# Performance work log

Hardware: AMD Instinct MI355X
Metric: run time of the kernel (lower is better)

## Reference

```python
import jax, jax.numpy as jnp
import numpy as np

EMBED_DIM = 256
NUM_HEADS = 4
LN_EPS = 1e-5


def setup_inputs() -> dict:
    b, n, e = 2, 4096, EMBED_DIM
    key = jax.random.key(0)
    ks = jax.random.split(key, 12)
    x = jax.random.normal(ks[0], (b, n, e), dtype=jnp.float32)
    # rotary cache: cos/sin of random angles, shape [2, b, n, e, 1]
    ang = jax.random.uniform(ks[1], (b, n, e, 1), dtype=jnp.float32) * (2 * np.pi)
    encoding = jnp.stack([jnp.cos(ang), jnp.sin(ang)], axis=0)
    s_e = 1.0 / np.sqrt(e)
    s_2e = 1.0 / np.sqrt(2 * e)
    Wqkv_w = jax.random.normal(ks[2], (3 * e, e), dtype=jnp.float32) * s_e
    Wqkv_b = jax.random.normal(ks[3], (3 * e,), dtype=jnp.float32) * s_e
    out_w = jax.random.normal(ks[4], (e, e), dtype=jnp.float32) * s_e
    out_b = jax.random.normal(ks[5], (e,), dtype=jnp.float32) * s_e
    ffn1_w = jax.random.normal(ks[6], (2 * e, 2 * e), dtype=jnp.float32) * s_2e
    ffn1_b = jax.random.normal(ks[7], (2 * e,), dtype=jnp.float32) * s_2e
    ln_g = jnp.ones((2 * e,), dtype=jnp.float32)
    ln_b = jnp.zeros((2 * e,), dtype=jnp.float32)
    ffn2_w = jax.random.normal(ks[8], (e, 2 * e), dtype=jnp.float32) * s_2e
    ffn2_b = jax.random.normal(ks[9], (e,), dtype=jnp.float32) * s_2e
    return {"x": x, "encoding": encoding, "Wqkv_w": Wqkv_w, "Wqkv_b": Wqkv_b,
            "out_w": out_w, "out_b": out_b, "ffn1_w": ffn1_w, "ffn1_b": ffn1_b,
            "ln_g": ln_g, "ln_b": ln_b, "ffn2_w": ffn2_w, "ffn2_b": ffn2_b}


def _forward(x, encoding, Wqkv_w, Wqkv_b, out_w, out_b, ffn1_w, ffn1_b, ln_g, ln_b, ffn2_w, ffn2_b):
    b, n, e = x.shape
    h = NUM_HEADS
    hd = e // h
    qkv = x @ Wqkv_w.T + Wqkv_b                      # [b,n,3e]
    qkv = qkv.reshape(b, n, e, 3)
    qk, v = qkv[..., :2], qkv[..., 2]                # [b,n,e,2], [b,n,e]
    # rotate_half: interpret e as (h, hd//2, 2) pairs, rotate within pairs
    r = qk.reshape(b, n, h, hd // 2, 2, 2)
    r = jnp.stack([-r[..., 1, :], r[..., 0, :]], axis=4).reshape(b, n, e, 2)
    qk = qk * encoding[0] + r * encoding[1]          # cached rotary emb
    q = qk[..., 0].reshape(b, n, h, hd)
    k = qk[..., 1].reshape(b, n, h, hd)
    vh = v.reshape(b, n, h, hd)
    scale = 1.0 / np.sqrt(hd).astype(np.float32)
    scores = jnp.einsum('bqhd,bkhd->bhqk', q, k) * scale
    attn = jax.nn.softmax(scores, axis=-1)
    ctx = jnp.einsum('bhqk,bkhd->bqhd', attn, vh).reshape(b, n, e)
    message = ctx @ out_w.T + out_b
    y = jnp.concatenate([x, message], axis=2)        # [b,n,2e]
    y = y @ ffn1_w.T + ffn1_b
    mu = jnp.mean(y, axis=-1, keepdims=True)
    var = jnp.mean(jnp.square(y - mu), axis=-1, keepdims=True)
    y = (y - mu) * jax.lax.rsqrt(var + LN_EPS) * ln_g + ln_b
    y = jax.nn.gelu(y, approximate=False)            # torch nn.GELU default = exact
    y = y @ ffn2_w.T + ffn2_b
    return x + y


def reference(x, encoding, Wqkv_w, Wqkv_b, out_w, out_b, ffn1_w, ffn1_b, ln_g, ln_b, ffn2_w, ffn2_b):
    return _forward(x, encoding, Wqkv_w, Wqkv_b, out_w, out_b, ffn1_w, ffn1_b, ln_g, ln_b, ffn2_w, ffn2_b)
```

## Files before the change

kernel.cpp:

```cpp
#include <hip/hip_runtime.h>
#include <hip/hip_bf16.h>

using u16 = unsigned short;
using u16x8 = __attribute__((ext_vector_type(8))) unsigned short;
using s16x4 = __attribute__((ext_vector_type(4))) short;
using s16x8 = __attribute__((ext_vector_type(8))) short;
using f32x4 = __attribute__((ext_vector_type(4))) float;

__device__ __forceinline__ f32x4 mfma16(s16x8 a, s16x8 b, f32x4 c) {
    return __builtin_amdgcn_mfma_f32_16x16x32_bf16(a, b, c, 0, 0, 0);
}

__device__ __forceinline__ u16 f2bf(float f) {
    union { float f; unsigned u; } v; v.f = f;
    unsigned r = v.u + 0x7FFFu + ((v.u >> 16) & 1u);
    return (u16)(r >> 16);
}

__device__ __forceinline__ unsigned cvt_pk_bf16(float lo, float hi) {
    unsigned r;
    asm("v_cvt_pk_bf16_f32 %0, %1, %2" : "=v"(r) : "v"(lo), "v"(hi));
    return r;
}

__device__ __forceinline__ float fast_exp2(float x) {
    float r;
    asm("v_exp_f32 %0, %1" : "=v"(r) : "v"(x));
    return r;
}

__device__ __forceinline__ unsigned pk2(u16 a, u16 b) {
    return (unsigned)a | ((unsigned)b << 16);
}

__device__ __forceinline__ float bf2f(u16 u) {
    union { unsigned u; float f; } v; v.u = ((unsigned)u) << 16;
    return v.f;
}

__device__ __forceinline__ void gload_lds16(const u16* g, u16* l) {
    __builtin_amdgcn_global_load_lds(
        (const __attribute__((address_space(1))) void*)g,
        (__attribute__((address_space(3))) void*)l, 16, 0, 0);
}

__global__ __launch_bounds__(256) void conv_kernel(
    const float* __restrict__ s0, const float* __restrict__ s1,
    const float* __restrict__ s2, const float* __restrict__ s3,
    const float* __restrict__ s4,
    u16* __restrict__ d0, u16* __restrict__ d1, u16* __restrict__ d2,
    u16* __restrict__ d3, u16* __restrict__ d4)
{
    int i = blockIdx.x * 256 + threadIdx.x;
    const float* s; u16* d; int off;
    if (i < 524288)      { s = s0; d = d0; off = i; }
    else if (i < 573440) { s = s1; d = d1; off = i - 524288; }
    else if (i < 589824) { s = s2; d = d2; off = i - 573440; }
    else if (i < 655360) { s = s3; d = d3; off = i - 589824; }
    else                 { s = s4; d = d4; off = i - 655360; }
    float4 f = ((const float4*)s)[off];
    ushort4 u;
    u.x = f2bf(f.x); u.y = f2bf(f.y); u.z = f2bf(f.z); u.w = f2bf(f.w);
    ((ushort4*)d)[off] = u;
}

template<int OUTMODE, bool SPLIT, bool RESID, int BM>
__global__ __launch_bounds__(256) void gemm_kernel(
    const u16* __restrict__ A0, const u16* __restrict__ A1,
    const u16* __restrict__ W, const float* __restrict__ bias,
    const float* __restrict__ resid, float* __restrict__ outf,
    u16* __restrict__ outb, int M, int N, int K)
{
    constexpr int MS = BM / 32;
    __shared__ u16 A_lds[3][BM][64];
    __shared__ u16 B_lds[3][64][64];
    const int tid = threadIdx.x;
    const int l = tid & 63, w = tid >> 6;
    const int lr = l & 15, lg = l >> 4;
    const int r7 = lr & 7;
    const int m0 = blockIdx.x * BM, n0 = blockIdx.y * 64;
    const int wm = (w >> 1) * (BM / 2), wn = (w & 1) * 32;

    const int lrow = l >> 3;
    const int swz = (l & 7) ^ lrow;
    const int arow = (BM / 4) * w + lrow;
    const int brow = 16 * w + lrow;

    #define STAGE_G(s, b)                                                     \
        do {                                                                  \
            int k0_ = 64 * (s);                                               \
            const u16* As_; int lda_;                                         \
            if (SPLIT) {                                                      \
                lda_ = 256;                                                   \
                As_ = (k0_ < 256) ? (A0 + k0_) : (A1 + (k0_ - 256));          \
            } else { lda_ = K; As_ = A0 + k0_; }                              \
            _Pragma("unroll")                                                 \
            for (int i = 0; i < BM / 32; ++i)                                 \
                gload_lds16(As_ + (size_t)(m0 + arow + 8 * i) * lda_ + swz * 8,\
                            &A_lds[b][(BM / 4) * w + 8 * i][0]);              \
            _Pragma("unroll")                                                 \
            for (int i = 0; i < 2; ++i)                                       \
                gload_lds16(W + (size_t)(n0 + brow + 8 * i) * K + k0_ + swz * 8,\
                            &B_lds[b][16 * w + 8 * i][0]);                    \
        } while (0)

    f32x4 acc[MS][2];
    #pragma unroll
    for (int i = 0; i < MS; ++i)
        #pragma unroll
        for (int j = 0; j < 2; ++j)
            acc[i][j] = (f32x4){0.f, 0.f, 0.f, 0.f};

    const int NS = K >> 6;
    int cur = 0, nxt = 1;
    STAGE_G(0, 0);

    for (int s = 0; s < NS; ++s) {
        if (s + 1 < NS) {
            STAGE_G(s + 1, nxt);
            if constexpr (BM == 128)
                asm volatile("s_waitcnt vmcnt(6)" ::: "memory");
            else
                asm volatile("s_waitcnt vmcnt(4)" ::: "memory");
        } else {
            asm volatile("s_waitcnt vmcnt(0)" ::: "memory");
        }
        __builtin_amdgcn_sched_barrier(0);
        __builtin_amdgcn_s_barrier();
        __builtin_amdgcn_sched_barrier(0);

        #pragma unroll
        for (int ks = 0; ks < 2; ++ks) {
            s16x8 af[MS], bfr[2];
            #pragma unroll
            for (int ms = 0; ms < MS; ++ms)
                af[ms] = *(const s16x8*)&A_lds[cur][wm + ms * 16 + lr]
                                              [((ks * 4 + lg) ^ r7) * 8];
            #pragma unroll
            for (int ns = 0; ns < 2; ++ns)
                bfr[ns] = *(const s16x8*)&B_lds[cur][wn + ns * 16 + lr]
                                               [((ks * 4 + lg) ^ r7) * 8];
            #pragma unroll
            for (int ms = 0; ms < MS; ++ms)
                #pragma unroll
                for (int ns = 0; ns < 2; ++ns)
                    acc[ms][ns] = mfma16(af[ms], bfr[ns], acc[ms][ns]);
        }
        cur = nxt;
        nxt = (nxt == 2) ? 0 : nxt + 1;
    }
    #undef STAGE_G

    #pragma unroll
    for (int ms = 0; ms < MS; ++ms) {
        #pragma unroll
        for (int ns = 0; ns < 2; ++ns) {
            int cg = n0 + wn + ns * 16 + lr;
            float bv = bias[cg];
            #pragma unroll
            for (int r = 0; r < 4; ++r) {
                int rg = m0 + wm + ms * 16 + lg * 4 + r;
                float val = acc[ms][ns][r] + bv;
                if (RESID) val += resid[(size_t)rg * N + cg];
                if (OUTMODE == 0) outf[(size_t)rg * N + cg] = val;
                else              outb[(size_t)rg * N + cg] = f2bf(val);
            }
        }
    }
}

__global__ __launch_bounds__(256) void rope_kernel(
    const u16* __restrict__ qkv, const float* __restrict__ enc,
    u16* __restrict__ Qo, u16* __restrict__ Ko, u16* __restrict__ Vo)
{
    int idx = blockIdx.x * 256 + threadIdx.x;
    int row = idx >> 7;
    int p = idx & 127;
    int c0 = p * 2;
    const u16* base = qkv + (size_t)row * 768 + p * 6;
    ushort2 a01 = *(const ushort2*)(base);
    ushort2 a23 = *(const ushort2*)(base + 2);
    ushort2 a45 = *(const ushort2*)(base + 4);
    float q0 = bf2f(a01.x), k0 = bf2f(a01.y);
    float q1 = bf2f(a23.y), k1 = bf2f(a45.x);
    const float* cb = enc + (size_t)row * 256 + c0;
    float2 cosv = *(const float2*)cb;
    float2 sinv = *(const float2*)(cb + 2097152);
    float qr0 = q0 * cosv.x - q1 * sinv.x;
    float qr1 = q1 * cosv.y + q0 * sinv.y;
    float kr0 = k0 * cosv.x - k1 * sinv.x;
    float kr1 = k1 * cosv.y + k0 * sinv.y;
    const float qs = 0.18033688011112042f;
    qr0 *= qs; qr1 *= qs;
    int h = c0 >> 6, d = c0 & 63;
    int b = row >> 12, n = row & 4095;
    size_t o = (((size_t)(b * 4 + h)) * 4096 + n) * 64 + d;
    *(unsigned*)(Qo + o) = cvt_pk_bf16(qr0, qr1);
    *(unsigned*)(Ko + o) = cvt_pk_bf16(kr0, kr1);
    *(unsigned*)(Vo + o) = pk2(a23.x, a45.y);
}

__global__ __launch_bounds__(256) void transpose_v(
    const u16* __restrict__ V, u16* __restrict__ Vt)
{
    __shared__ u16 t[64][72];
    int bh = blockIdx.y, n0 = blockIdx.x * 64;
    int tid = threadIdx.x;
    #pragma unroll
    for (int i = 0; i < 2; ++i) {
        int c = tid + 256 * i;
        int r = c >> 3, cg = c & 7;
        *(uint4*)&t[r][cg * 8] =
            *(const uint4*)(V + ((size_t)bh * 4096 + n0 + r) * 64 + cg * 8);
    }
    __syncthreads();
    #pragma unroll
    for (int i = 0; i < 2; ++i) {
        int c = tid + 256 * i;
        int d = c >> 3, ng = c & 7;
        int kb = ng >> 2, lg4 = ng & 3;
        int base = 32 * kb + 4 * lg4;
        unsigned w0 = pk2(t[base +  0][d], t[base +  1][d]);
        unsigned w1 = pk2(t[base +  2][d], t[base +  3][d]);
        unsigned w2 = pk2(t[base + 16][d], t[base + 17][d]);
        unsigned w3 = pk2(t[base + 18][d], t[base + 19][d]);
        uint4 o4 = make_uint4(w0, w1, w2, w3);
        *(uint4*)(Vt + ((size_t)bh * 64 + d) * 4096 + n0 + ng * 8) = o4;
    }
}

__global__ __launch_bounds__(256) void attn_kernel(
    const u16* __restrict__ Qp, const u16* __restrict__ Kp,
    const u16* __restrict__ Vtp, u16* __restrict__ Opart,
    float* __restrict__ Ssum)
{
    __shared__ u16 K_lds[2][64][64];
    __shared__ u16 V_lds[2][64][64];
    const int tid = threadIdx.x;
    const int l = tid & 63, w = tid >> 6;
    const int lr = l & 15, lg = l >> 4;
    const int r7 = lr & 7;
    const int bh = blockIdx.y, z = blockIdx.z;
    const int n0 = blockIdx.x * 128 + w * 32;

    const u16* Qb = Qp + ((size_t)bh * 4096 + n0) * 64;
    s16x8 qf[2][2];
    #pragma unroll
    for (int qt = 0; qt < 2; ++qt)
        #pragma unroll
        for (int dh = 0; dh < 2; ++dh)
            qf[qt][dh] = *(const s16x8*)(Qb + (qt * 16 + lr) * 64 + dh * 32 + lg * 8);

    const u16* Kb = Kp + (size_t)bh * 4096 * 64 + (size_t)z * 1024 * 64;
    const u16* Vb = Vtp + (size_t)bh * 64 * 4096 + z * 1024;

    const int xs0 = (lg ^ r7) * 8;
    const int xs1 = ((4 + lg) ^ r7) * 8;

    const int swz = (l & 7) ^ ((l >> 3) & 7);
    const int row0 = 16 * w + (l >> 3);
    const size_t koff0 = (size_t)row0 * 64 + swz * 8;
    const size_t koff1 = (size_t)(row0 + 8) * 64 + swz * 8;
    const size_t voff0 = (size_t)row0 * 4096 + swz * 8;
    const size_t voff1 = (size_t)(row0 + 8) * 4096 + swz * 8;

    #define STAGE(kt, b)                                                      \
        do {                                                                  \
            const u16* ks_ = Kb + (size_t)(kt) * 4096;                        \
            const u16* vs_ = Vb + (size_t)(kt) * 64;                          \
            gload_lds16(ks_ + koff0, &K_lds[b][16 * w][0]);                   \
            gload_lds16(ks_ + koff1, &K_lds[b][16 * w + 8][0]);               \
            gload_lds16(vs_ + voff0, &V_lds[b][16 * w][0]);                   \
            gload_lds16(vs_ + voff1, &V_lds[b][16 * w + 8][0]);               \
        } while (0)

    f32x4 O[2][4];
    #pragma unroll
    for (int qt = 0; qt < 2; ++qt)
        #pragma unroll
        for (int dv = 0; dv < 4; ++dv)
            O[qt][dv] = (f32x4){0.f, 0.f, 0.f, 0.f};
    f32x4 ssum[2];
    ssum[0] = (f32x4){0.f, 0.f, 0.f, 0.f};
    ssum[1] = (f32x4){0.f, 0.f, 0.f, 0.f};
    s16x8 ones;
    #pragma unroll
    for (int j = 0; j < 8; ++j) ones[j] = (short)0x3F80;

    STAGE(0, 0);
    __syncthreads();

    #define PHASE(kt, CB, DO_STAGE)                                           \
        do {                                                                  \
            if (DO_STAGE) STAGE((kt) + 1, (CB) ^ 1);                          \
            f32x4 S[2][4];                                                    \
            __builtin_amdgcn_s_setprio(1);                                    \
            _Pragma("unroll")                                                 \
            for (int v4 = 0; v4 < 4; ++v4) {                                  \
                const int krow = v4 * 16 + lr;                                \
                s16x8 kf0 = *(const s16x8*)&K_lds[CB][krow][xs0];             \
                s16x8 kf1 = *(const s16x8*)&K_lds[CB][krow][xs1];             \
                _Pragma("unroll")                                             \
                for (int qt = 0; qt < 2; ++qt) {                              \
                    f32x4 zz = (f32x4){-24.f, -24.f, -24.f, -24.f};           \
                    zz = mfma16(kf0, qf[qt][0], zz);                          \
                    zz = mfma16(kf1, qf[qt][1], zz);                          \
                    S[qt][v4] = zz;                                           \
                }                                                             \
            }                                                                 \
            __builtin_amdgcn_s_setprio(0);                                    \
            s16x8 pa[2][2];                                                   \
            _Pragma("unroll")                                                 \
            for (int qt = 0; qt < 2; ++qt) {                                  \
                float p[4][4];                                                \
                _Pragma("unroll")                                             \
                for (int v4 = 0; v4 < 4; ++v4)                                \
                    _Pragma("unroll")                                         \
                    for (int r = 0; r < 4; ++r)                               \
                        p[v4][r] = fast_exp2(S[qt][v4][r]);                   \
                _Pragma("unroll")                                             \
                for (int kb = 0; kb < 2; ++kb) {                              \
                    union { unsigned u[4]; s16x8 v; } pu;                     \
                    pu.u[0] = cvt_pk_bf16(p[2*kb][0],   p[2*kb][1]);          \
                    pu.u[1] = cvt_pk_bf16(p[2*kb][2],   p[2*kb][3]);          \
                    pu.u[2] = cvt_pk_bf16(p[2*kb+1][0], p[2*kb+1][1]);        \
                    pu.u[3] = cvt_pk_bf16(p[2*kb+1][2], p[2*kb+1][3]);        \
                    pa[qt][kb] = pu.v;                                        \
                }                                                             \
            }                                                                 \
            __builtin_amdgcn_s_setprio(1);                                    \
            _Pragma("unroll")                                                 \
            for (int dv = 0; dv < 4; ++dv) {                                  \
                const int vrow = 16 * dv + lr;                                \
                s16x8 vf0 = *(const s16x8*)&V_lds[CB][vrow][xs0];             \
                s16x8 vf1 = *(const s16x8*)&V_lds[CB][vrow][xs1];             \
                _Pragma("unroll")                                             \
                for (int qt = 0; qt < 2; ++qt) {                              \
                    O[qt][dv] = mfma16(pa[qt][0], vf0, O[qt][dv]);            \
                    O[qt][dv] = mfma16(pa[qt][1], vf1, O[qt][dv]);            \
                }                                                             \
            }                                                                 \
            _Pragma("unroll")                                                 \
            for (int qt = 0; qt < 2; ++qt) {                                  \
                ssum[qt] = mfma16(pa[qt][0], ones, ssum[qt]);                 \
                ssum[qt] = mfma16(pa[qt][1], ones, ssum[qt]);                 \
            }                                                                 \
            __builtin_amdgcn_s_setprio(0);                                    \
            __syncthreads();                                                  \
        } while (0)

    #pragma unroll 1
    for (int kt = 0; kt < 16; kt += 2) {
        PHASE(kt, 0, true);
        PHASE(kt + 1, 1, kt < 14);
    }
    #undef PHASE
    #undef STAGE

    u16* Ob = Opart + ((size_t)(z * 8 + bh) * 4096 + n0) * 64;
    #pragma unroll
    for (int qt = 0; qt < 2; ++qt)
        #pragma unroll
        for (int dv = 0; dv < 4; ++dv)
            #pragma unroll
            for (int r = 0; r < 4; ++r)
                Ob[(size_t)(qt * 16 + 4 * lg + r) * 64 + 16 * dv + lr] =
                    f2bf(O[qt][dv][r]);
    if (lr == 0) {
        #pragma unroll
        for (int qt = 0; qt < 2; ++qt) {
            float4 sv = make_float4(ssum[qt][0], ssum[qt][1],
                                    ssum[qt][2], ssum[qt][3]);
            *(float4*)&Ssum[(size_t)(z * 8 + bh) * 4096 + n0 + qt * 16 + 4 * lg] = sv;
        }
    }
}

__global__ __launch_bounds__(256) void combine_kernel(
    const u16* __restrict__ Opart, const float* __restrict__ Ssum,
    u16* __restrict__ ctx)
{
    int idx = blockIdx.x * 256 + threadIdx.x;
    int rr = idx >> 3;
    int dc = (idx & 7) * 8;
    float s = Ssum[rr] + Ssum[32768 + rr] + Ssum[65536 + rr] + Ssum[98304 + rr];
    float inv = 1.f / s;
    float acc[8];
    #pragma unroll
    for (int j = 0; j < 8; ++j) acc[j] = 0.f;
    #pragma unroll
    for (int z = 0; z < 4; ++z) {
        u16x8 ov = *(const u16x8*)(Opart + ((size_t)z * 32768 + rr) * 64 + dc);
        #pragma unroll
        for (int j = 0; j < 8; ++j) acc[j] += bf2f(ov[j]);
    }
    #pragma unroll
    for (int j = 0; j < 8; ++j) acc[j] *= inv;
    int bh = rr >> 12, n = rr & 4095;
    int b = bh >> 2, h = bh & 3;
    uint4 o4 = make_uint4(cvt_pk_bf16(acc[0], acc[1]), cvt_pk_bf16(acc[2], acc[3]),
                          cvt_pk_bf16(acc[4], acc[5]), cvt_pk_bf16(acc[6], acc[7]));
    *(uint4*)(ctx + ((size_t)(b * 4096 + n)) * 256 + h * 64 + dc) = o4;
}

__global__ __launch_bounds__(256) void ln_gelu_kernel(
    const float* __restrict__ y, const float* __restrict__ g,
    const float* __restrict__ bta, u16* __restrict__ o)
{
    int row = blockIdx.x * 4 + (threadIdx.x >> 6);
    int l = threadIdx.x & 63;
    const float* yr = y + (size_t)row * 512 + l * 8;
    float4 va = *(const float4*)yr;
    float4 vb = *(const float4*)(yr + 4);
    float v[8] = {va.x, va.y, va.z, va.w, vb.x, vb.y, vb.z, vb.w};
    float s = 0.f;
    #pragma unroll
    for (int j = 0; j < 8; ++j) s += v[j];
    #pragma unroll
    for (int off = 32; off; off >>= 1) s += __shfl_xor(s, off, 64);
    float mu = s * (1.f / 512.f);
    float q = 0.f;
    #pragma unroll
    for (int j = 0; j < 8; ++j) { float t = v[j] - mu; q += t * t; }
    #pragma unroll
    for (int off = 32; off; off >>= 1) q += __shfl_xor(q, off, 64);
    float rs = rsqrtf(q * (1.f / 512.f) + 1e-5f);
    u16 u[8];
    #pragma unroll
    for (int j = 0; j < 8; ++j) {
        float t = (v[j] - mu) * rs * g[l * 8 + j] + bta[l * 8 + j];
        t = t * 0.5f * (1.f + erff(t * 0.70710678118654752f));
        u[j] = f2bf(t);
    }
    uint4 o4 = make_uint4(pk2(u[0], u[1]), pk2(u[2], u[3]),
                          pk2(u[4], u[5]), pk2(u[6], u[7]));
    *(uint4*)(o + (size_t)row * 512 + l * 8) = o4;
}

extern "C" void kernel_launch(void* const* d_in, const int* in_sizes, int n_in,
                              void* d_out, int out_size, void* d_ws, size_t ws_size,
                              hipStream_t stream) {
    (void)in_sizes; (void)n_in; (void)out_size; (void)ws_size;
    const float* x    = (const float*)d_in[0];
    const float* enc  = (const float*)d_in[1];
    const float* wqkv = (const float*)d_in[2];
    const float* bqkv = (const float*)d_in[3];
    const float* wout = (const float*)d_in[4];
    const float* bout = (const float*)d_in[5];
    const float* w1   = (const float*)d_in[6];
    const float* b1   = (const float*)d_in[7];
    const float* lng  = (const float*)d_in[8];
    const float* lnb  = (const float*)d_in[9];
    const float* w2   = (const float*)d_in[10];
    const float* b2   = (const float*)d_in[11];
    float* out = (float*)d_out;
    char* ws = (char*)d_ws;

    u16*   xb    = (u16*)(ws + 0);
    u16*   wqkvb = (u16*)(ws + 4194304);
    u16*   woutb = (u16*)(ws + 4587520);
    u16*   w1b   = (u16*)(ws + 4718592);
    u16*   w2b   = (u16*)(ws + 5242880);
    u16*   qkvb  = (u16*)(ws + 5505024);
    u16*   OpartB= (u16*)(ws + 5505024);
    float* y1    = (float*)(ws + 5505024);
    float* Ssum  = (float*)(ws + 22282240);
    u16*   q     = (u16*)(ws + 30670848);
    u16*   k     = (u16*)(ws + 34865152);
    u16*   v     = (u16*)(ws + 39059456);
    u16*   vt    = (u16*)(ws + 43253760);
    u16*   ybf   = q;
    u16*   ctx   = (u16*)(ws + 47448064);
    u16*   msg   = (u16*)(ws + 51642368);

    conv_kernel<<<2688, 256, 0, stream>>>(x, wqkv, wout, w1, w2,
                                          xb, wqkvb, woutb, w1b, w2b);
    gemm_kernel<1, false, false, 128><<<dim3(64, 12), 256, 0, stream>>>(
        xb, nullptr, wqkvb, bqkv, nullptr, nullptr, qkvb, 8192, 768, 256);
    rope_kernel<<<4096, 256, 0, stream>>>(qkvb, enc, q, k, v);
    transpose_v<<<dim3(64, 8), 256, 0, stream>>>(v, vt);
    attn_kernel<<<dim3(32, 8, 4), 256, 0, stream>>>(q, k, vt, OpartB, Ssum);
    combine_kernel<<<1024, 256, 0, stream>>>(OpartB, Ssum, ctx);
    gemm_kernel<1, false, false, 64><<<dim3(128, 4), 256, 0, stream>>>(
        ctx, nullptr, woutb, bout, nullptr, nullptr, msg, 8192, 256, 256);
    gemm_kernel<0, true, false, 128><<<dim3(64, 8), 256, 0, stream>>>(
        xb, msg, w1b, b1, nullptr, y1, nullptr, 8192, 512, 512);
    ln_gelu_kernel<<<2048, 256, 0, stream>>>(y1, lng, lnb, ybf);
    gemm_kernel<0, false, true, 64><<<dim3(128, 4), 256, 0, stream>>>(
        ybf, nullptr, w2b, b2, x, out, nullptr, 8192, 256, 512);
}
```

Before: 124.3 us.

## Fold out-projection into FFN1 weights, fuse rope with V transpose, store FFN1 output bf16

The out-projection GEMM is removed by precomputing W1[:,256:] @ Wout as a combined weight and folding out_b into the FFN1 bias. FFN1 then reads ctx directly, using a split-K over both A and W. The rope kernel now writes V transposed through LDS, which removes the separate transpose kernel and the V buffer. The FFN1 output is stored as bf16 instead of fp32 to halve LN traffic. This adds a small weight-prep GEMM and bias kernel, plus extra bf16 rounding of the fused weight and of the pre-LN activations.

Result: slower. 132.9 us (+6.8%).

```diff
diff --git a/kernel.cpp b/kernel.cpp
--- a/kernel.cpp
+++ b/kernel.cpp
@@ -64,12 +64,55 @@
     ((ushort4*)d)[off] = u;
 }
 
-template<int OUTMODE, bool SPLIT, bool RESID, int BM>
+__global__ __launch_bounds__(256) void prep_kernel(
+    const float* __restrict__ wout, const float* __restrict__ w1,
+    const float* __restrict__ outb, const float* __restrict__ b1,
+    u16* __restrict__ woutT, float* __restrict__ b1p)
+{
+    int bid = blockIdx.x, tid = threadIdx.x;
+    if (bid < 16) {
+        __shared__ u16 ts[64][72];
+        int tr = (bid >> 2) * 64, tc = (bid & 3) * 64;
+        #pragma unroll
+        for (int i = 0; i < 2; ++i) {
+            int c = tid + 256 * i;
+            int r = c >> 3, cg = c & 7;
+            float4 fa = *(const float4*)(wout + (size_t)(tr + r) * 256 + tc + cg * 8);
+            float4 fb = *(const float4*)(wout + (size_t)(tr + r) * 256 + tc + cg * 8 + 4);
+            ts[r][cg * 8 + 0] = f2bf(fa.x); ts[r][cg * 8 + 1] = f2bf(fa.y);
+            ts[r][cg * 8 + 2] = f2bf(fa.z); ts[r][cg * 8 + 3] = f2bf(fa.w);
+            ts[r][cg * 8 + 4] = f2bf(fb.x); ts[r][cg * 8 + 5] = f2bf(fb.y);
+            ts[r][cg * 8 + 6] = f2bf(fb.z); ts[r][cg * 8 + 7] = f2bf(fb.w);
+        }
+        __syncthreads();
+        #pragma unroll
+        for (int i = 0; i < 2; ++i) {
+            int c = tid + 256 * i;
+            int d = c >> 3, ng = c & 7;
+            uint4 o4 = make_uint4(
+                pk2(ts[ng*8+0][d], ts[ng*8+1][d]), pk2(ts[ng*8+2][d], ts[ng*8+3][d]),
+                pk2(ts[ng*8+4][d], ts[ng*8+5][d]), pk2(ts[ng*8+6][d], ts[ng*8+7][d]));
+            *(uint4*)(woutT + (size_t)(tc + d) * 256 + tr + ng * 8) = o4;
+        }
+    } else {
+        #pragma unroll
+        for (int h = 0; h < 2; ++h) {
+            int n = tid + 256 * h;
+            float acc = b1[n];
+            const float* wr = w1 + (size_t)n * 512 + 256;
+            for (int k = 0; k < 256; ++k) acc += wr[k] * outb[k];
+            b1p[n] = acc;
+        }
+    }
+}
+
+template<int OUTMODE, bool SPLIT, bool SPLITW, bool RESID, bool BIAS, int BM>
 __global__ __launch_bounds__(256) void gemm_kernel(
     const u16* __restrict__ A0, const u16* __restrict__ A1,
-    const u16* __restrict__ W, const float* __restrict__ bias,
-    const float* __restrict__ resid, float* __restrict__ outf,
-    u16* __restrict__ outb, int M, int N, int K)
+    const u16* __restrict__ W0, const u16* __restrict__ W1,
+    const float* __restrict__ bias, const float* __restrict__ resid,
+    float* __restrict__ outf, u16* __restrict__ outb,
+    int M, int N, int K, int lda0, int lda1, int ldw0, int ldw1, int ldo)
 {
     constexpr int MS = BM / 32;
     __shared__ u16 A_lds[3][BM][64];
@@ -89,18 +132,19 @@
     #define STAGE_G(s, b)                                                     \
         do {                                                                  \
             int k0_ = 64 * (s);                                               \
-            const u16* As_; int lda_;                                         \
-            if (SPLIT) {                                                      \
-                lda_ = 256;                                                   \
-                As_ = (k0_ < 256) ? (A0 + k0_) : (A1 + (k0_ - 256));          \
-            } else { lda_ = K; As_ = A0 + k0_; }                              \
+            const u16* As_; int lda_; int ka_ = k0_;                          \
+            if (SPLIT && k0_ >= 256) { As_ = A1; lda_ = lda1; ka_ = k0_ - 256; }\
+            else { As_ = A0; lda_ = lda0; }                                   \
+            const u16* Ws_; int ldw_; int kw_ = k0_;                          \
+            if (SPLITW && k0_ >= 256) { Ws_ = W1; ldw_ = ldw1; kw_ = k0_ - 256; }\
+            else { Ws_ = W0; ldw_ = ldw0; }                                   \
             _Pragma("unroll")                                                 \
             for (int i = 0; i < BM / 32; ++i)                                 \
-                gload_lds16(As_ + (size_t)(m0 + arow + 8 * i) * lda_ + swz * 8,\
+                gload_lds16(As_ + (size_t)(m0 + arow + 8 * i) * lda_ + ka_ + swz * 8,\
                             &A_lds[b][(BM / 4) * w + 8 * i][0]);              \
             _Pragma("unroll")                                                 \
             for (int i = 0; i < 2; ++i)                                       \
-                gload_lds16(W + (size_t)(n0 + brow + 8 * i) * K + k0_ + swz * 8,\
+                gload_lds16(Ws_ + (size_t)(n0 + brow + 8 * i) * ldw_ + kw_ + swz * 8,\
                             &B_lds[b][16 * w + 8 * i][0]);                    \
         } while (0)
 
@@ -156,62 +200,52 @@
         #pragma unroll
         for (int ns = 0; ns < 2; ++ns) {
             int cg = n0 + wn + ns * 16 + lr;
-            float bv = bias[cg];
+            float bv = BIAS ? bias[cg] : 0.f;
             #pragma unroll
             for (int r = 0; r < 4; ++r) {
                 int rg = m0 + wm + ms * 16 + lg * 4 + r;
                 float val = acc[ms][ns][r] + bv;
                 if (RESID) val += resid[(size_t)rg * N + cg];
-                if (OUTMODE == 0) outf[(size_t)rg * N + cg] = val;
-                else              outb[(size_t)rg * N + cg] = f2bf(val);
+                if (OUTMODE == 0) outf[(size_t)rg * ldo + cg] = val;
+                else              outb[(size_t)rg * ldo + cg] = f2bf(val);
             }
         }
     }
 }
 
-__global__ __launch_bounds__(256) void rope_kernel(
+__global__ __launch_bounds__(256) void rope_tv_kernel(
     const u16* __restrict__ qkv, const float* __restrict__ enc,
-    u16* __restrict__ Qo, u16* __restrict__ Ko, u16* __restrict__ Vo)
-{
-    int idx = blockIdx.x * 256 + threadIdx.x;
-    int row = idx >> 7;
-    int p = idx & 127;
-    int c0 = p * 2;
-    const u16* base = qkv + (size_t)row * 768 + p * 6;
-    ushort2 a01 = *(const ushort2*)(base);
-    ushort2 a23 = *(const ushort2*)(base + 2);
-    ushort2 a45 = *(const ushort2*)(base + 4);
-    float q0 = bf2f(a01.x), k0 = bf2f(a01.y);
-    float q1 = bf2f(a23.y), k1 = bf2f(a45.x);
-    const float* cb = enc + (size_t)row * 256 + c0;
-    float2 cosv = *(const float2*)cb;
-    float2 sinv = *(const float2*)(cb + 2097152);
-    float qr0 = q0 * cosv.x - q1 * sinv.x;
-    float qr1 = q1 * cosv.y + q0 * sinv.y;
-    float kr0 = k0 * cosv.x - k1 * sinv.x;
-    float kr1 = k1 * cosv.y + k0 * sinv.y;
+    u16* __restrict__ Qo, u16* __restrict__ Ko, u16* __restrict__ Vt)
+{
+    __shared__ u16 vt_lds[64][72];
+    const int tid = threadIdx.x;
+    const int bh = blockIdx.y, n0 = blockIdx.x * 64;
+    const int b = bh >> 2, h = bh & 3;
     const float qs = 0.18033688011112042f;
-    qr0 *= qs; qr1 *= qs;
-    int h = c0 >> 6, d = c0 & 63;
-    int b = row >> 12, n = row & 4095;
-    size_t o = (((size_t)(b * 4 + h)) * 4096 + n) * 64 + d;
-    *(unsigned*)(Qo + o) = cvt_pk_bf16(qr0, qr1);
-    *(unsigned*)(Ko + o) = cvt_pk_bf16(kr0, kr1);
-    *(unsigned*)(Vo + o) = pk2(a23.x, a45.y);
-}
-
-__global__ __launch_bounds__(256) void transpose_v(
-    const u16* __restrict__ V, u16* __restrict__ Vt)
-{
-    __shared__ u16 t[64][72];
-    int bh = blockIdx.y, n0 = blockIdx.x * 64;
-    int tid = threadIdx.x;
-    #pragma unroll
-    for (int i = 0; i < 2; ++i) {
-        int c = tid + 256 * i;
-        int r = c >> 3, cg = c & 7;
-        *(uint4*)&t[r][cg * 8] =
-            *(const uint4*)(V + ((size_t)bh * 4096 + n0 + r) * 64 + cg * 8);
+
+    #pragma unroll
+    for (int it = 0; it < 8; ++it) {
+        int task = it * 256 + tid;
+        int r = task >> 5, t = task & 31;
+        size_t grow = (size_t)(b * 4096 + n0 + r);
+        const u16* base = qkv + grow * 768 + 3 * (h * 64) + 6 * t;
+        ushort2 a01 = *(const ushort2*)(base);
+        ushort2 a23 = *(const ushort2*)(base + 2);
+        ushort2 a45 = *(const ushort2*)(base + 4);
+        float q0 = bf2f(a01.x), k0 = bf2f(a01.y);
+        float q1 = bf2f(a23.y), k1 = bf2f(a45.x);
+        const float* cb = enc + grow * 256 + h * 64 + 2 * t;
+        float2 cosv = *(const float2*)cb;
+        float2 sinv = *(const float2*)(cb + 2097152);
+        float qr0 = (q0 * cosv.x - q1 * sinv.x) * qs;
+        float qr1 = (q1 * cosv.y + q0 * sinv.y) * qs;
+        float kr0 = k0 * cosv.x - k1 * sinv.x;
+        float kr1 = k1 * cosv.y + k0 * sinv.y;
+        size_t o = ((size_t)bh * 4096 + n0 + r) * 64 + 2 * t;
+        *(unsigned*)(Qo + o) = cvt_pk_bf16(qr0, qr1);
+        *(unsigned*)(Ko + o) = cvt_pk_bf16(kr0, kr1);
+        vt_lds[r][2 * t]     = a23.x;
+        vt_lds[r][2 * t + 1] = a45.y;
     }
     __syncthreads();
     #pragma unroll
@@ -220,10 +254,10 @@
         int d = c >> 3, ng = c & 7;
         int kb = ng >> 2, lg4 = ng & 3;
         int base = 32 * kb + 4 * lg4;
-        unsigned w0 = pk2(t[base +  0][d], t[base +  1][d]);
-        unsigned w1 = pk2(t[base +  2][d], t[base +  3][d]);
-        unsigned w2 = pk2(t[base + 16][d], t[base + 17][d]);
-        unsigned w3 = pk2(t[base + 18][d], t[base + 19][d]);
+        unsigned w0 = pk2(vt_lds[base +  0][d], vt_lds[base +  1][d]);
+        unsigned w1 = pk2(vt_lds[base +  2][d], vt_lds[base +  3][d]);
+        unsigned w2 = pk2(vt_lds[base + 16][d], vt_lds[base + 17][d]);
+        unsigned w3 = pk2(vt_lds[base + 18][d], vt_lds[base + 19][d]);
         uint4 o4 = make_uint4(w0, w1, w2, w3);
         *(uint4*)(Vt + ((size_t)bh * 64 + d) * 4096 + n0 + ng * 8) = o4;
     }
@@ -404,15 +438,16 @@
 }
 
 __global__ __launch_bounds__(256) void ln_gelu_kernel(
-    const float* __restrict__ y, const float* __restrict__ g,
+    const u16* __restrict__ y, const float* __restrict__ g,
     const float* __restrict__ bta, u16* __restrict__ o)
 {
     int row = blockIdx.x * 4 + (threadIdx.x >> 6);
     int l = threadIdx.x & 63;
-    const float* yr = y + (size_t)row * 512 + l * 8;
-    float4 va = *(const float4*)yr;
-    float4 vb = *(const float4*)(yr + 4);
-    float v[8] = {va.x, va.y, va.z, va.w, vb.x, vb.y, vb.z, vb.w};
+    const u16* yr = y + (size_t)row * 512 + l * 8;
+    u16x8 uv = *(const u16x8*)yr;
+    float v[8];
+    #pragma unroll
+    for (int j = 0; j < 8; ++j) v[j] = bf2f(uv[j]);
     float s = 0.f;
     #pragma unroll
     for (int j = 0; j < 8; ++j) s += v[j];
@@ -463,29 +498,34 @@
     u16*   w2b   = (u16*)(ws + 5242880);
     u16*   qkvb  = (u16*)(ws + 5505024);
     u16*   OpartB= (u16*)(ws + 5505024);
-    float* y1    = (float*)(ws + 5505024);
+    u16*   y1bf  = (u16*)(ws + 5505024);
     float* Ssum  = (float*)(ws + 22282240);
+    u16*   woutT = (u16*)(ws + 22806528);
+    u16*   wprime= (u16*)(ws + 22937600);
+    float* b1p   = (float*)(ws + 23199744);
     u16*   q     = (u16*)(ws + 30670848);
     u16*   k     = (u16*)(ws + 34865152);
-    u16*   v     = (u16*)(ws + 39059456);
     u16*   vt    = (u16*)(ws + 43253760);
     u16*   ybf   = q;
     u16*   ctx   = (u16*)(ws + 47448064);
-    u16*   msg   = (u16*)(ws + 51642368);
 
     conv_kernel<<<2688, 256, 0, stream>>>(x, wqkv, wout, w1, w2,
                                           xb, wqkvb, woutb, w1b, w2b);
-    gemm_kernel<1, false, false, 128><<<dim3(64, 12), 256, 0, stream>>>(
-        xb, nullptr, wqkvb, bqkv, nullptr, nullptr, qkvb, 8192, 768, 256);
-    rope_kernel<<<4096, 256, 0, stream>>>(qkvb, enc, q, k, v);
-    transpose_v<<<dim3(64, 8), 256, 0, stream>>>(v, vt);
+    prep_kernel<<<17, 256, 0, stream>>>(wout, w1, bout, b1, woutT, b1p);
+    gemm_kernel<1, false, false, false, false, 64><<<dim3(8, 4), 256, 0, stream>>>(
+        w1b + 256, nullptr, woutT, nullptr, nullptr, nullptr, nullptr, wprime,
+        512, 256, 256, 512, 0, 256, 0, 256);
+    gemm_kernel<1, false, false, false, true, 128><<<dim3(64, 12), 256, 0, stream>>>(
+        xb, nullptr, wqkvb, nullptr, bqkv, nullptr, nullptr, qkvb,
+        8192, 768, 256, 256, 0, 256, 0, 768);
+    rope_tv_kernel<<<dim3(64, 8), 256, 0, stream>>>(qkvb, enc, q, k, vt);
     attn_kernel<<<dim3(32, 8, 4), 256, 0, stream>>>(q, k, vt, OpartB, Ssum);
     combine_kernel<<<1024, 256, 0, stream>>>(OpartB, Ssum, ctx);
-    gemm_kernel<1, false, false, 64><<<dim3(128, 4), 256, 0, stream>>>(
-        ctx, nullptr, woutb, bout, nullptr, nullptr, msg, 8192, 256, 256);
-    gemm_kernel<0, true, false, 128><<<dim3(64, 8), 256, 0, stream>>>(
-        xb, msg, w1b, b1, nullptr, y1, nullptr, 8192, 512, 512);
-    ln_gelu_kernel<<<2048, 256, 0, stream>>>(y1, lng, lnb, ybf);
-    gemm_kernel<0, false, true, 64><<<dim3(128, 4), 256, 0, stream>>>(
-        ybf, nullptr, w2b, b2, x, out, nullptr, 8192, 256, 512);
-}
+    gemm_kernel<1, true, true, false, true, 128><<<dim3(64, 8), 256, 0, stream>>>(
+        xb, ctx, w1b, wprime, b1p, nullptr, nullptr, y1bf,
+        8192, 512, 512, 256, 256, 512, 256, 512);
+    ln_gelu_kernel<<<2048, 256, 0, stream>>>(y1bf, lng, lnb, ybf);
+    gemm_kernel<0, false, false, true, true, 64><<<dim3(128, 4), 256, 0, stream>>>(
+        ybf, nullptr, w2b, nullptr, b2, x, out, nullptr,
+        8192, 256, 512, 512, 0, 512, 0, 256);
+}
```
